# Optimization experiments

Hardware: AMD Instinct MI355X
Metric: run time of the kernel (lower is better)

The kernel has to match this reference:

```python
import jax, jax.numpy as jnp
import numpy as np

NUM_HEAD = 8
HEAD_DIM = 64
TEMPERATURE = 10000.0


def positional_encoding(L, D):
    # Mirrors get_positional_encoding: sin on even-indexed, cos on odd-indexed
    # columns of pos, interleaved via stack+reshape.
    embed = jnp.arange(L, dtype=jnp.float32)
    dim_t = jnp.arange(D, dtype=jnp.float32)
    dim_t = TEMPERATURE ** (2.0 * jnp.floor(dim_t / 2.0) / D)
    pos = embed[:, None] / dim_t                      # [L, D]
    pos = jnp.stack([jnp.sin(pos[:, 0::2]), jnp.cos(pos[:, 1::2])], axis=2)
    return pos.reshape(1, L, D)                       # [1, L, D]


def setup_inputs() -> dict:
    key = jax.random.key(0)
    ks = jax.random.split(key, 4)
    B, L, D = 8, 1024, 256
    HD = NUM_HEAD * HEAD_DIM                          # 512
    glorot = float(np.sqrt(2.0 / (D + HD)))
    return {
        "x": jax.random.normal(ks[0], (B, L, D), jnp.float32),
        "Wq": jax.random.normal(ks[1], (D, HD), jnp.float32) * glorot,
        "bq": jnp.zeros((NUM_HEAD,), jnp.float32),
        "Wk": jax.random.normal(ks[2], (D, HD), jnp.float32) * glorot,
        "bk": jnp.zeros((NUM_HEAD,), jnp.float32),
        "Wv": jax.random.normal(ks[3], (D, HD), jnp.float32) * glorot,
        "bv": jnp.zeros((NUM_HEAD,), jnp.float32),
    }


def reference(x, Wq, bq, Wk, bk, Wv, bv):
    B, L, D = x.shape
    pe = positional_encoding(L, D)
    qk_in = x + pe                                    # query/key get pos-enc, value does not
    # per-head bias broadcast over head_dim (tf.repeat(bias, head_dim))
    q = qk_in @ Wq + jnp.repeat(bq, HEAD_DIM)
    k = qk_in @ Wk + jnp.repeat(bk, HEAD_DIM)
    v = x @ Wv + jnp.repeat(bv, HEAD_DIM)
    split = lambda t: t.reshape(B, L, NUM_HEAD, HEAD_DIM)
    q, k, v = split(q), split(k), split(v)
    att = jnp.einsum('blhd,bmhd->bhlm', q, k) * (float(HEAD_DIM) ** -0.5)
    att = jax.nn.softmax(att, axis=-1)                # [B, H, L, L]
    out = jnp.einsum('bhlm,bmhd->blhd', att, v)       # [B, L, H, hd]
    return out.reshape(B, L, NUM_HEAD * HEAD_DIM)
```

## Files before the change

### kernel.cpp

```cpp
#include <hip/hip_runtime.h>
#include <hip/hip_bf16.h>

#define NB   8
#define NL   1024
#define ND   256
#define NH   8
#define NHD  64
#define NC   512
#define NTOK (NB*NL)

typedef __bf16 bf16x8v __attribute__((ext_vector_type(8)));
typedef float f32x4 __attribute__((ext_vector_type(4)));

__device__ __forceinline__ unsigned short f2bf(float f) {
  unsigned u = __float_as_uint(f);
  unsigned r = (u + 0x7fffu + ((u >> 16) & 1u)) >> 16;
  return (unsigned short)r;
}

__device__ __forceinline__ unsigned pack_bf16x2(float lo, float hi) {
  __hip_bfloat162 h2 = __float22bfloat162_rn(make_float2(lo, hi));
  union { __hip_bfloat162 h; unsigned u; } cvt;
  cvt.h = h2;
  return cvt.u;
}

__global__ __launch_bounds__(256) void prep_kernel(
    const float* __restrict__ x,
    const float* __restrict__ Wq, const float* __restrict__ Wk,
    const float* __restrict__ Wv,
    unsigned short* __restrict__ xpe, unsigned short* __restrict__ xb,
    unsigned short* __restrict__ wqt, unsigned short* __restrict__ wkt,
    unsigned short* __restrict__ wvt) {
  const int bid = blockIdx.x;
  const int tid = threadIdx.x;
  if (bid < (NTOK * ND) / (256 * 8)) {
    int idx = bid * 256 + tid;
    int d0 = (idx & 31) * 8;
    int t = idx >> 5;
    int l = t & (NL - 1);
    float4 xa = *(const float4*)(x + (size_t)t * ND + d0);
    float4 xc = *(const float4*)(x + (size_t)t * ND + d0 + 4);
    float xv[8] = {xa.x, xa.y, xa.z, xa.w, xc.x, xc.y, xc.z, xc.w};
    unsigned short pe_out[8], xb_out[8];
#pragma unroll
    for (int p = 0; p < 4; ++p) {
      float inv_dim = __expf(-0.07195578415606394f * (float)(d0 / 2 + p));
      float ang = (float)l * inv_dim;
      float sv = __sinf(ang);
      float cv = __cosf(ang);
      pe_out[2 * p]     = f2bf(xv[2 * p] + sv);
      pe_out[2 * p + 1] = f2bf(xv[2 * p + 1] + cv);
      xb_out[2 * p]     = f2bf(xv[2 * p]);
      xb_out[2 * p + 1] = f2bf(xv[2 * p + 1]);
    }
    *(int4*)(xpe + (size_t)t * ND + d0) = *(int4*)pe_out;
    *(int4*)(xb  + (size_t)t * ND + d0) = *(int4*)xb_out;
  } else {
    __shared__ float tile[64 * 65];
    int widx = bid - (NTOK * ND) / (256 * 8);
    int m = widx >> 5;
    int tl = widx & 31;
    int kt = tl & 3;
    int nt = tl >> 2;
    const float* W = (m == 0) ? Wq : (m == 1) ? Wk : Wv;
    unsigned short* Wt = (m == 0) ? wqt : (m == 1) ? wkt : wvt;
    int c = tid & 63, rb = tid >> 6;
#pragma unroll
    for (int i = 0; i < 16; ++i) {
      int r = i * 4 + rb;
      tile[r * 65 + c] = W[(kt * 64 + r) * NC + nt * 64 + c];
    }
    __syncthreads();
#pragma unroll
    for (int i = 0; i < 16; ++i) {
      int n_local = i * 4 + rb, k_local = c;
      Wt[(nt * 64 + n_local) * ND + kt * 64 + k_local] =
          f2bf(tile[k_local * 65 + n_local]);
    }
  }
}

__global__ __launch_bounds__(256) void gemm_qkv_kernel(
    const unsigned short* __restrict__ xpe, const unsigned short* __restrict__ xb,
    const unsigned short* __restrict__ wqt, const unsigned short* __restrict__ wkt,
    const unsigned short* __restrict__ wvt,
    const float* __restrict__ bq, const float* __restrict__ bk,
    const float* __restrict__ bv,
    unsigned short* __restrict__ qg, unsigned short* __restrict__ kg,
    unsigned short* __restrict__ vg) {
  __shared__ unsigned short As[128 * 72];
  __shared__ unsigned short Bs[64 * 72];

  const int z = blockIdx.z;
  const unsigned short* X  = (z == 2) ? xb : xpe;
  const unsigned short* Wt = (z == 0) ? wqt : (z == 1) ? wkt : wvt;
  const float* bias        = (z == 0) ? bq  : (z == 1) ? bk  : bv;
  unsigned short* Out      = (z == 0) ? qg  : (z == 1) ? kg  : vg;
  const float scale        = (z == 0) ? 0.18033688011112042f : 1.0f;

  const int nt = blockIdx.x;
  const int mt = blockIdx.y;
  const int tid = threadIdx.x;
  const int w = tid >> 6;
  const int lane = tid & 63;
  const int lg = lane >> 4;
  const int lr = lane & 15;

  const int r0 = tid >> 3;
  const int c8o = (tid & 7) * 8;
  const unsigned short* Abase = X + (size_t)(mt * 128 + r0) * ND + c8o;
  const unsigned short* Bbase = Wt + (size_t)(nt * 64 + r0) * ND + c8o;
  unsigned short* Adst = As + r0 * 72 + c8o;
  unsigned short* Bdst = Bs + r0 * 72 + c8o;

  f32x4 acc[2][4] = {};
  int4 a0, a1, a2, a3, b0, b1;

#define GLOADS(kb)                                              \
  a0 = *(const int4*)(Abase + (kb) * 64);                       \
  a1 = *(const int4*)(Abase + (kb) * 64 + 32 * ND);             \
  a2 = *(const int4*)(Abase + (kb) * 64 + 64 * ND);             \
  a3 = *(const int4*)(Abase + (kb) * 64 + 96 * ND);             \
  b0 = *(const int4*)(Bbase + (kb) * 64);                       \
  b1 = *(const int4*)(Bbase + (kb) * 64 + 32 * ND);

  GLOADS(0)
#pragma unroll
  for (int kb = 0; kb < 4; ++kb) {
    if (kb) __syncthreads();
    *(int4*)(Adst)           = a0;
    *(int4*)(Adst + 32 * 72) = a1;
    *(int4*)(Adst + 64 * 72) = a2;
    *(int4*)(Adst + 96 * 72) = a3;
    *(int4*)(Bdst)           = b0;
    *(int4*)(Bdst + 32 * 72) = b1;
    if (kb == 0) { GLOADS(1) }
    else if (kb == 1) { GLOADS(2) }
    else if (kb == 2) { GLOADS(3) }
    __syncthreads();

#pragma unroll
    for (int kk = 0; kk < 2; ++kk) {
      bf16x8v a[2], b[4];
#pragma unroll
      for (int mi = 0; mi < 2; ++mi)
        a[mi] = *(const bf16x8v*)(As + (w * 32 + mi * 16 + lr) * 72 + kk * 32 + lg * 8);
#pragma unroll
      for (int nb = 0; nb < 4; ++nb)
        b[nb] = *(const bf16x8v*)(Bs + (nb * 16 + lr) * 72 + kk * 32 + lg * 8);
#pragma unroll
      for (int mi = 0; mi < 2; ++mi)
#pragma unroll
        for (int nb = 0; nb < 4; ++nb)
          acc[mi][nb] = __builtin_amdgcn_mfma_f32_16x16x32_bf16(
              a[mi], b[nb], acc[mi][nb], 0, 0, 0);
    }
  }
#undef GLOADS

#pragma unroll
  for (int mi = 0; mi < 2; ++mi) {
#pragma unroll
    for (int nb = 0; nb < 4; ++nb) {
#pragma unroll
      for (int j = 0; j < 4; ++j) {
        int r = mt * 128 + w * 32 + mi * 16 + lg * 4 + j;
        int c = nt * 64 + nb * 16 + lr;
        int bb = r >> 10, lpos = r & (NL - 1);
        int h = c >> 6, dd = c & 63;
        float val = (acc[mi][nb][j] + bias[h]) * scale;
        if (z < 2)
          Out[((bb * NH + h) * NL + lpos) * NHD + dd] = f2bf(val);
        else
          Out[((bb * NH + h) * NHD + dd) * NL + lpos] = f2bf(val);
      }
    }
  }
}

__global__ __launch_bounds__(256) void attn_kernel(
    const unsigned short* __restrict__ Q,
    const unsigned short* __restrict__ K,
    const unsigned short* __restrict__ Vt,
    float* __restrict__ Out) {
  __shared__ unsigned short Ks[64 * 72];
  __shared__ unsigned short Vs[64 * 72];
  __shared__ unsigned short Ps[64 * 72];

  const int qt = blockIdx.x;
  const int bh = blockIdx.y;
  const int bb = bh >> 3, h = bh & 7;
  const int tid = threadIdx.x;
  const int w = tid >> 6;
  const int lane = tid & 63;
  const int lg = lane >> 4, lr = lane & 15;
  const int qrow0 = qt * 64 + w * 16;

  bf16x8v qf[2];
#pragma unroll
  for (int kk = 0; kk < 2; ++kk)
    qf[kk] = *(const bf16x8v*)(Q + ((size_t)bh * NL + qrow0 + lr) * NHD + kk * 32 + lg * 8);

  const int r0 = tid >> 3;
  const int c8o = (tid & 7) * 8;
  const unsigned short* kp0 = K + (size_t)bh * NL * NHD + r0 * NHD + c8o;
  const unsigned short* vp0 = Vt + ((size_t)bh * NHD + r0) * NL + c8o;
  unsigned short* kdst = Ks + r0 * 72 + c8o;
  unsigned short* vdst = Vs + r0 * 72 + c8o;

  float m_ = -1e30f, lsum = 0.0f;
  f32x4 o[4] = {};
  int4 ka, kc, va, vc;

#define KVLOADS(kv)                                             \
  ka = *(const int4*)(kp0 + (kv) * 64 * NHD);                   \
  kc = *(const int4*)(kp0 + (kv) * 64 * NHD + 32 * NHD);        \
  va = *(const int4*)(vp0 + (kv) * 64);                         \
  vc = *(const int4*)(vp0 + (kv) * 64 + 32 * NL);

  KVLOADS(0)
  for (int kv = 0; kv < 16; ++kv) {
    if (kv) __syncthreads();
    *(int4*)(kdst)           = ka;
    *(int4*)(kdst + 32 * 72) = kc;
    *(int4*)(vdst)           = va;
    *(int4*)(vdst + 32 * 72) = vc;
    if (kv < 15) { KVLOADS(kv + 1) }
    __syncthreads();

    f32x4 s[4] = {};
#pragma unroll
    for (int kk = 0; kk < 2; ++kk) {
#pragma unroll
      for (int nb = 0; nb < 4; ++nb) {
        bf16x8v kf = *(const bf16x8v*)(Ks + (nb * 16 + lr) * 72 + kk * 32 + lg * 8);
        s[nb] = __builtin_amdgcn_mfma_f32_16x16x32_bf16(kf, qf[kk], s[nb], 0, 0, 0);
      }
    }

    float tm = s[0][0];
#pragma unroll
    for (int nb = 0; nb < 4; ++nb)
#pragma unroll
      for (int j = 0; j < 4; ++j) tm = fmaxf(tm, s[nb][j]);
    tm = fmaxf(tm, __shfl_xor(tm, 16, 64));
    tm = fmaxf(tm, __shfl_xor(tm, 32, 64));
    if (__any(tm > m_ + 8.0f)) {
      float nm = fmaxf(m_, tm);
      float corr = exp2f(m_ - nm);
      m_ = nm;
      lsum *= corr;
#pragma unroll
      for (int db = 0; db < 4; ++db)
#pragma unroll
        for (int j = 0; j < 4; ++j) o[db][j] *= corr;
    }
    float ts = 0.0f;
#pragma unroll
    for (int nb = 0; nb < 4; ++nb)
#pragma unroll
      for (int j = 0; j < 4; ++j) {
        float p = exp2f(s[nb][j] - m_);
        s[nb][j] = p;
        ts += p;
      }
    ts += __shfl_xor(ts, 16, 64);
    ts += __shfl_xor(ts, 32, 64);
    lsum += ts;

#pragma unroll
    for (int nb = 0; nb < 4; ++nb)
#pragma unroll
      for (int hh = 0; hh < 2; ++hh)
        *(unsigned*)(Ps + (w * 16 + lr) * 72 + nb * 16 + lg * 4 + 2 * hh) =
            pack_bf16x2(s[nb][2 * hh], s[nb][2 * hh + 1]);

#pragma unroll
    for (int kk = 0; kk < 2; ++kk) {
      bf16x8v pf = *(const bf16x8v*)(Ps + (w * 16 + lr) * 72 + kk * 32 + lg * 8);
#pragma unroll
      for (int db = 0; db < 4; ++db) {
        bf16x8v vf = *(const bf16x8v*)(Vs + (db * 16 + lr) * 72 + kk * 32 + lg * 8);
        o[db] = __builtin_amdgcn_mfma_f32_16x16x32_bf16(vf, pf, o[db], 0, 0, 0);
      }
    }
  }
#undef KVLOADS

  float inv = 1.0f / lsum;
  int q = qrow0 + lr;
#pragma unroll
  for (int db = 0; db < 4; ++db) {
    f32x4 ov;
#pragma unroll
    for (int j = 0; j < 4; ++j) ov[j] = o[db][j] * inv;
    *(f32x4*)(Out + (size_t)(bb * NL + q) * NC + h * NHD + db * 16 + lg * 4) = ov;
  }
}

extern "C" void kernel_launch(void* const* d_in, const int* in_sizes, int n_in,
                              void* d_out, int out_size, void* d_ws, size_t ws_size,
                              hipStream_t stream) {
  const float* x  = (const float*)d_in[0];
  const float* Wq = (const float*)d_in[1];
  const float* bq = (const float*)d_in[2];
  const float* Wk = (const float*)d_in[3];
  const float* bk = (const float*)d_in[4];
  const float* Wv = (const float*)d_in[5];
  const float* bv = (const float*)d_in[6];
  float* out = (float*)d_out;

  unsigned short* xpe = (unsigned short*)d_ws;
  unsigned short* xb  = xpe + (size_t)NTOK * ND;
  unsigned short* wqt = xb  + (size_t)NTOK * ND;
  unsigned short* wkt = wqt + (size_t)ND * NC;
  unsigned short* wvt = wkt + (size_t)ND * NC;
  unsigned short* qg  = wvt + (size_t)ND * NC;
  unsigned short* kg  = qg  + (size_t)NB * NH * NL * NHD;
  unsigned short* vg  = kg  + (size_t)NB * NH * NL * NHD;

  int prep_blocks = (NTOK * ND) / (256 * 8) + 96;
  prep_kernel<<<prep_blocks, 256, 0, stream>>>(x, Wq, Wk, Wv, xpe, xb, wqt, wkt, wvt);

  gemm_qkv_kernel<<<dim3(8, 64, 3), 256, 0, stream>>>(
      xpe, xb, wqt, wkt, wvt, bq, bk, bv, qg, kg, vg);

  attn_kernel<<<dim3(16, 64), 256, 0, stream>>>(qg, kg, vg, out);
}
```

Baseline: 142.3 us.

## Enlarge QKV GEMM tile to 128x128 and add MFMA priority hints in attention

The QKV projection GEMM now computes a 128x128 output tile per block with a 2x2 wave layout, so each wave holds a 64x64 accumulator. This halves the grid along N and increases operand reuse per LDS load, at the cost of more registers and more shared memory. The attention kernel wraps its MFMA sections in s_setprio hints and rewrites the row max and sum reductions as trees to shorten dependency chains.

Measured after the change: 137.9 us. -3.1%, faster.

```diff
diff --git a/kernel.cpp b/kernel.cpp
--- a/kernel.cpp
+++ b/kernel.cpp
@@ -90,7 +90,7 @@
     unsigned short* __restrict__ qg, unsigned short* __restrict__ kg,
     unsigned short* __restrict__ vg) {
   __shared__ unsigned short As[128 * 72];
-  __shared__ unsigned short Bs[64 * 72];
+  __shared__ unsigned short Bs[128 * 72];
 
   const int z = blockIdx.z;
   const unsigned short* X  = (z == 2) ? xb : xpe;
@@ -103,6 +103,7 @@
   const int mt = blockIdx.y;
   const int tid = threadIdx.x;
   const int w = tid >> 6;
+  const int wm = w >> 1, wn = w & 1;
   const int lane = tid & 63;
   const int lg = lane >> 4;
   const int lr = lane & 15;
@@ -110,12 +111,12 @@
   const int r0 = tid >> 3;
   const int c8o = (tid & 7) * 8;
   const unsigned short* Abase = X + (size_t)(mt * 128 + r0) * ND + c8o;
-  const unsigned short* Bbase = Wt + (size_t)(nt * 64 + r0) * ND + c8o;
+  const unsigned short* Bbase = Wt + (size_t)(nt * 128 + r0) * ND + c8o;
   unsigned short* Adst = As + r0 * 72 + c8o;
   unsigned short* Bdst = Bs + r0 * 72 + c8o;
 
-  f32x4 acc[2][4] = {};
-  int4 a0, a1, a2, a3, b0, b1;
+  f32x4 acc[4][4] = {};
+  int4 a0, a1, a2, a3, b0, b1, b2, b3;
 
 #define GLOADS(kb)                                              \
   a0 = *(const int4*)(Abase + (kb) * 64);                       \
@@ -123,7 +124,9 @@
   a2 = *(const int4*)(Abase + (kb) * 64 + 64 * ND);             \
   a3 = *(const int4*)(Abase + (kb) * 64 + 96 * ND);             \
   b0 = *(const int4*)(Bbase + (kb) * 64);                       \
-  b1 = *(const int4*)(Bbase + (kb) * 64 + 32 * ND);
+  b1 = *(const int4*)(Bbase + (kb) * 64 + 32 * ND);             \
+  b2 = *(const int4*)(Bbase + (kb) * 64 + 64 * ND);             \
+  b3 = *(const int4*)(Bbase + (kb) * 64 + 96 * ND);
 
   GLOADS(0)
 #pragma unroll
@@ -135,6 +138,8 @@
     *(int4*)(Adst + 96 * 72) = a3;
     *(int4*)(Bdst)           = b0;
     *(int4*)(Bdst + 32 * 72) = b1;
+    *(int4*)(Bdst + 64 * 72) = b2;
+    *(int4*)(Bdst + 96 * 72) = b3;
     if (kb == 0) { GLOADS(1) }
     else if (kb == 1) { GLOADS(2) }
     else if (kb == 2) { GLOADS(3) }
@@ -142,34 +147,35 @@
 
 #pragma unroll
     for (int kk = 0; kk < 2; ++kk) {
-      bf16x8v a[2], b[4];
-#pragma unroll
-      for (int mi = 0; mi < 2; ++mi)
-        a[mi] = *(const bf16x8v*)(As + (w * 32 + mi * 16 + lr) * 72 + kk * 32 + lg * 8);
-#pragma unroll
-      for (int nb = 0; nb < 4; ++nb)
-        b[nb] = *(const bf16x8v*)(Bs + (nb * 16 + lr) * 72 + kk * 32 + lg * 8);
-#pragma unroll
-      for (int mi = 0; mi < 2; ++mi)
-#pragma unroll
-        for (int nb = 0; nb < 4; ++nb)
-          acc[mi][nb] = __builtin_amdgcn_mfma_f32_16x16x32_bf16(
-              a[mi], b[nb], acc[mi][nb], 0, 0, 0);
+      bf16x8v a[4], b[4];
+#pragma unroll
+      for (int mi = 0; mi < 4; ++mi)
+        a[mi] = *(const bf16x8v*)(As + (wm * 64 + mi * 16 + lr) * 72 + kk * 32 + lg * 8);
+#pragma unroll
+      for (int nj = 0; nj < 4; ++nj)
+        b[nj] = *(const bf16x8v*)(Bs + (wn * 64 + nj * 16 + lr) * 72 + kk * 32 + lg * 8);
+#pragma unroll
+      for (int mi = 0; mi < 4; ++mi)
+#pragma unroll
+        for (int nj = 0; nj < 4; ++nj)
+          acc[mi][nj] = __builtin_amdgcn_mfma_f32_16x16x32_bf16(
+              a[mi], b[nj], acc[mi][nj], 0, 0, 0);
     }
   }
 #undef GLOADS
 
-#pragma unroll
-  for (int mi = 0; mi < 2; ++mi) {
-#pragma unroll
-    for (int nb = 0; nb < 4; ++nb) {
+  const float bval = bias[nt * 2 + wn];
+  const int h = nt * 2 + wn;
+#pragma unroll
+  for (int mi = 0; mi < 4; ++mi) {
+#pragma unroll
+    for (int nj = 0; nj < 4; ++nj) {
 #pragma unroll
       for (int j = 0; j < 4; ++j) {
-        int r = mt * 128 + w * 32 + mi * 16 + lg * 4 + j;
-        int c = nt * 64 + nb * 16 + lr;
+        int r = mt * 128 + wm * 64 + mi * 16 + lg * 4 + j;
+        int dd = nj * 16 + lr;
         int bb = r >> 10, lpos = r & (NL - 1);
-        int h = c >> 6, dd = c & 63;
-        float val = (acc[mi][nb][j] + bias[h]) * scale;
+        float val = (acc[mi][nj][j] + bval) * scale;
         if (z < 2)
           Out[((bb * NH + h) * NL + lpos) * NHD + dd] = f2bf(val);
         else
@@ -230,6 +236,7 @@
     __syncthreads();
 
     f32x4 s[4] = {};
+    __builtin_amdgcn_s_setprio(1);
 #pragma unroll
     for (int kk = 0; kk < 2; ++kk) {
 #pragma unroll
@@ -238,12 +245,18 @@
         s[nb] = __builtin_amdgcn_mfma_f32_16x16x32_bf16(kf, qf[kk], s[nb], 0, 0, 0);
       }
     }
-
-    float tm = s[0][0];
-#pragma unroll
-    for (int nb = 0; nb < 4; ++nb)
-#pragma unroll
-      for (int j = 0; j < 4; ++j) tm = fmaxf(tm, s[nb][j]);
+    __builtin_amdgcn_s_setprio(0);
+
+    float tm;
+    {
+      float a0 = fmaxf(s[0][0], s[0][1]), a1 = fmaxf(s[0][2], s[0][3]);
+      float a2 = fmaxf(s[1][0], s[1][1]), a3 = fmaxf(s[1][2], s[1][3]);
+      float a4 = fmaxf(s[2][0], s[2][1]), a5 = fmaxf(s[2][2], s[2][3]);
+      float a6 = fmaxf(s[3][0], s[3][1]), a7 = fmaxf(s[3][2], s[3][3]);
+      float c0 = fmaxf(fmaxf(a0, a1), fmaxf(a2, a3));
+      float c1 = fmaxf(fmaxf(a4, a5), fmaxf(a6, a7));
+      tm = fmaxf(c0, c1);
+    }
     tm = fmaxf(tm, __shfl_xor(tm, 16, 64));
     tm = fmaxf(tm, __shfl_xor(tm, 32, 64));
     if (__any(tm > m_ + 8.0f)) {
@@ -256,15 +269,19 @@
 #pragma unroll
         for (int j = 0; j < 4; ++j) o[db][j] *= corr;
     }
-    float ts = 0.0f;
 #pragma unroll
     for (int nb = 0; nb < 4; ++nb)
 #pragma unroll
-      for (int j = 0; j < 4; ++j) {
-        float p = exp2f(s[nb][j] - m_);
-        s[nb][j] = p;
-        ts += p;
-      }
+      for (int j = 0; j < 4; ++j)
+        s[nb][j] = exp2f(s[nb][j] - m_);
+    float ts;
+    {
+      float a0 = s[0][0] + s[0][1], a1 = s[0][2] + s[0][3];
+      float a2 = s[1][0] + s[1][1], a3 = s[1][2] + s[1][3];
+      float a4 = s[2][0] + s[2][1], a5 = s[2][2] + s[2][3];
+      float a6 = s[3][0] + s[3][1], a7 = s[3][2] + s[3][3];
+      ts = ((a0 + a1) + (a2 + a3)) + ((a4 + a5) + (a6 + a7));
+    }
     ts += __shfl_xor(ts, 16, 64);
     ts += __shfl_xor(ts, 32, 64);
     lsum += ts;
@@ -276,6 +293,7 @@
         *(unsigned*)(Ps + (w * 16 + lr) * 72 + nb * 16 + lg * 4 + 2 * hh) =
             pack_bf16x2(s[nb][2 * hh], s[nb][2 * hh + 1]);
 
+    __builtin_amdgcn_s_setprio(1);
 #pragma unroll
     for (int kk = 0; kk < 2; ++kk) {
       bf16x8v pf = *(const bf16x8v*)(Ps + (w * 16 + lr) * 72 + kk * 32 + lg * 8);
@@ -285,6 +303,7 @@
         o[db] = __builtin_amdgcn_mfma_f32_16x16x32_bf16(vf, pf, o[db], 0, 0, 0);
       }
     }
+    __builtin_amdgcn_s_setprio(0);
   }
 #undef KVLOADS
 
@@ -323,7 +342,7 @@
   int prep_blocks = (NTOK * ND) / (256 * 8) + 96;
   prep_kernel<<<prep_blocks, 256, 0, stream>>>(x, Wq, Wk, Wv, xpe, xb, wqt, wkt, wvt);
 
-  gemm_qkv_kernel<<<dim3(8, 64, 3), 256, 0, stream>>>(
+  gemm_qkv_kernel<<<dim3(4, 64, 3), 256, 0, stream>>>(
       xpe, xb, wqt, wkt, wvt, bq, bk, bv, qg, kg, vg);
 
   attn_kernel<<<dim3(16, 64), 256, 0, stream>>>(qg, kg, vg, out);
```
